# Performance work log

Hardware: AMD Instinct MI355X
Metric: run time of the kernel (lower is better)

The kernel has to match this reference:

```python
import jax, jax.numpy as jnp
import numpy as np

B, N, M, Q, H, D = 1, 512, 512, 128, 8, 16
CLIP = 10.0

def _xavier(key, shape):
    # xavier_uniform over last two dims (fan_in=Q, fan_out=D per head)
    fan_in, fan_out = shape[-2], shape[-1]
    limit = float(np.sqrt(6.0 / (fan_in + fan_out)))
    return jax.random.uniform(key, shape, jnp.float32, -limit, limit)

def setup_inputs() -> dict:
    key = jax.random.key(0)
    ks = jax.random.split(key, 12)
    return {
        "x": jax.random.normal(ks[0], (B, N, Q), jnp.float32),
        "y": jax.random.normal(ks[1], (B, M, Q), jnp.float32),
        "z": jax.random.normal(ks[2], (B, N, M, Q), jnp.float32),
        "mask": jax.random.randint(ks[3], (B, N, M), 0, 2, jnp.int32),
        "lambda_x": _xavier(ks[4], (H, Q, D)),
        "lambda_y": _xavier(ks[5], (H, Q, D)),
        "lambda_z1": _xavier(ks[6], (H, Q, D)),
        "lambda_z2": _xavier(ks[7], (H, Q, D)),
        "bias_lambda_x": jnp.zeros((H, D), jnp.float32),
        "bias_lambda_y": jnp.zeros((H, D), jnp.float32),
        "theta1": _xavier(ks[8], (H, Q, D)),
        "theta2": _xavier(ks[9], (H, Q, D)),
        "bias_theta": jnp.zeros((H, D), jnp.float32),
    }

def reference(x, y, z, mask, lambda_x, lambda_y, lambda_z1, lambda_z2,
              bias_lambda_x, bias_lambda_y, theta1, theta2, bias_theta):
    head_dim = lambda_x.shape[-1]
    # node projections: [B,N,H,D] / [B,M,H,D]
    r_x = jnp.einsum('bnq,hqd->bnhd', x, lambda_x) + bias_lambda_x
    r_y = jnp.einsum('bmq,hqd->bmhd', y, lambda_y) + bias_lambda_y
    # edge projections: [B,N,M,H,D]
    r_z1 = jnp.einsum('bnmq,hqd->bnmhd', z, lambda_z1)
    r_z2 = jnp.einsum('bnmq,hqd->bnmhd', z, lambda_z2)
    # broadcast-add node + edge terms, dot over D -> scores [B,H,N,M]
    att = jnp.einsum('bnmhd,bnmhd->bhnm',
                     r_x[:, :, None, :, :] + r_z1,
                     r_y[:, None, :, :, :] + r_z2)
    att = att * (head_dim ** -0.5)
    att = CLIP * jnp.tanh(att)
    att = jnp.where(mask[:, None, :, :] == 1, -jnp.inf, att)
    # NOTE: softmax over the N (source) axis, matching torch dim=-2
    w = jax.nn.softmax(att, axis=-2)
    x_p = jnp.einsum('bnq,hqd->bnhd', x, theta1)
    r = jnp.einsum('bhnm,bnhd->bmhd', w, x_p) + bias_theta
    return jnp.einsum('bmhd,hqd->bmq', r, theta2)
```

## Files before the change

### kernel.cpp

```cpp
#include <hip/hip_runtime.h>
#include <hip/hip_bf16.h>
#include <math.h>

typedef __attribute__((ext_vector_type(8))) short short8;
typedef __attribute__((ext_vector_type(4))) float f32x4;

#define NT 8

__global__ void pack_kernel(const float* __restrict__ lz1,
                            const float* __restrict__ lz2,
                            const float* __restrict__ th2,
                            const float* __restrict__ bth,
                            const float* __restrict__ lx,
                            const float* __restrict__ ly,
                            const float* __restrict__ t1,
                            __hip_bfloat16* __restrict__ Wh,
                            __hip_bfloat16* __restrict__ Wl,
                            float* __restrict__ T2,
                            float* __restrict__ ob,
                            float* __restrict__ Lp) {
    int tid = blockIdx.x * blockDim.x + threadIdx.x;
    int stride = gridDim.x * blockDim.x;
    for (int i = tid; i < 256 * 128; i += stride) {
        int op = i >> 7, q = i & 127;
        int h = op >> 5, wh = (op >> 4) & 1, d = op & 15;
        float v = (wh ? lz2 : lz1)[(h * 128 + q) * 16 + d];
        __hip_bfloat16 hb = __float2bfloat16(v);
        Wh[i] = hb;
        Wl[i] = __float2bfloat16(v - __bfloat162float(hb));
    }
    for (int i = tid; i < 128 * 128; i += stride) {
        int o = i >> 7, q = i & 127;
        int h = o >> 4, d = o & 15;
        T2[i] = th2[(h * 128 + q) * 16 + d];
    }
    for (int i = tid; i < 3 * 128 * 128; i += stride) {
        int which = i >> 14, q = (i >> 7) & 127, o = i & 127;
        int h = o >> 4, d = o & 15;
        const float* S = (which == 0) ? lx : (which == 1) ? ly : t1;
        Lp[i] = S[(h * 128 + q) * 16 + d];
    }
    if (tid < 128) {
        int q = tid;
        float s = 0.f;
#pragma unroll
        for (int h = 0; h < 8; ++h) {
#pragma unroll
            for (int c = 0; c < 4; ++c) {
                float4 a = *(const float4*)&bth[h * 16 + c * 4];
                float4 b = *(const float4*)&th2[(h * 128 + q) * 16 + c * 4];
                s += a.x * b.x + a.y * b.y + a.z * b.z + a.w * b.w;
            }
        }
        ob[q] = s;
    }
}

__global__ __launch_bounds__(128) void proj_kernel(const float* __restrict__ x,
                            const float* __restrict__ y,
                            const float* __restrict__ Lp,
                            const float* __restrict__ blx,
                            const float* __restrict__ bly,
                            float* __restrict__ rx,
                            float* __restrict__ ry,
                            float* __restrict__ xp) {
    __shared__ float rows[4][128];
    const int n0 = blockIdx.x * 4;
    const int which = blockIdx.y;
    const float* in = (which == 1) ? y : x;
    const float* L  = Lp + which * 16384;
    const int o = threadIdx.x;
#pragma unroll
    for (int j = 0; j < 4; ++j)
        rows[j][o] = in[(n0 + j) * 128 + o];
    __syncthreads();
    float acc[4] = {0.f, 0.f, 0.f, 0.f};
#pragma unroll 4
    for (int q = 0; q < 128; ++q) {
        float wv = L[q * 128 + o];
#pragma unroll
        for (int j = 0; j < 4; ++j)
            acc[j] = fmaf(rows[j][q], wv, acc[j]);
    }
    float b = (which == 0) ? blx[o] : (which == 1) ? bly[o] : 0.f;
    float* dst = (which == 0) ? rx : (which == 1) ? ry : xp;
#pragma unroll
    for (int j = 0; j < 4; ++j)
        dst[(n0 + j) * 128 + o] = acc[j] + b;
}

__global__ __launch_bounds__(256, 2) void big_kernel(
        const float* __restrict__ z,
        const int* __restrict__ mask,
        const __hip_bfloat16* __restrict__ Wh,
        const __hip_bfloat16* __restrict__ Wl,
        const float* __restrict__ rx,
        const float* __restrict__ ry,
        float* __restrict__ w) {
    __shared__ short zsh[2][64 * 128];
    __shared__ short zsl[2][64 * 128];
    const int m0 = blockIdx.x * 64;
    const int n0 = blockIdx.y * NT;
    const int tid = threadIdx.x;
    const int og = tid >> 6;
    const int l  = tid & 63;
    const int lg = l >> 4;
    const int lm = l & 15;

    const int srow = tid >> 2, kseg = tid & 3;
    const float* zbase = &z[(size_t)(m0 + srow) * 128 + kseg * 32];

    short8 bhr[2][4][2];
#pragma unroll
    for (int p = 0; p < 2; ++p)
#pragma unroll
        for (int ks = 0; ks < 4; ++ks)
#pragma unroll
            for (int j = 0; j < 2; ++j)
                bhr[p][ks][j] = *(const short8*)&Wh[(size_t)(og * 64 + (p * 2 + j) * 16 + lm) * 128 + ks * 32 + lg * 8];

    float4 ryr[2][4];
#pragma unroll
    for (int p = 0; p < 2; ++p)
#pragma unroll
        for (int i = 0; i < 4; ++i)
            ryr[p][i] = *(const float4*)&ry[(size_t)(m0 + i * 16 + lm) * 128 + (og * 2 + p) * 16 + lg * 4];

    float4 zr[8];
#define LOADZ(nn)                                                         \
    {                                                                     \
        const float* p_ = zbase + (size_t)(nn) * 65536;                   \
        _Pragma("unroll")                                                 \
        for (int c_ = 0; c_ < 8; ++c_) zr[c_] = *(const float4*)&p_[c_ * 4]; \
    }

#define CONVERT_WRITE(b)                                                  \
    {                                                                     \
        _Pragma("unroll")                                                 \
        for (int c8 = 0; c8 < 4; ++c8) {                                  \
            float vv[8] = {zr[2 * c8].x, zr[2 * c8].y, zr[2 * c8].z, zr[2 * c8].w, \
                           zr[2 * c8 + 1].x, zr[2 * c8 + 1].y, zr[2 * c8 + 1].z, zr[2 * c8 + 1].w}; \
            union { short8 s; __hip_bfloat16 h[8]; } uh, ul;              \
            _Pragma("unroll")                                             \
            for (int jj = 0; jj < 8; ++jj) {                              \
                float f_ = vv[jj];                                        \
                __hip_bfloat16 hb_ = __float2bfloat16(f_);                \
                uh.h[jj] = hb_;                                           \
                ul.h[jj] = __float2bfloat16(f_ - __bfloat162float(hb_));  \
            }                                                             \
            int cw_ = (kseg * 4 + c8) ^ (srow & 7);                       \
            *(short8*)&zsh[b][srow * 128 + cw_ * 8] = uh.s;               \
            *(short8*)&zsl[b][srow * 128 + cw_ * 8] = ul.s;               \
        }                                                                 \
    }

    LOADZ(n0);
    CONVERT_WRITE(0);
    LOADZ(n0 + 1);
    __syncthreads();

    for (int t = 0; t < NT; ++t) {
        const int n = n0 + t;
        const int cur = t & 1;
        const int mk = mask[n * 512 + m0 + l];

#pragma unroll
        for (int p = 0; p < 2; ++p) {
            const int h = og * 2 + p;
            f32x4 acc[4][2];
#pragma unroll
            for (int i = 0; i < 4; ++i) {
                acc[i][0] = (f32x4){0.f, 0.f, 0.f, 0.f};
                acc[i][1] = (f32x4){0.f, 0.f, 0.f, 0.f};
            }
#pragma unroll
            for (int ks = 0; ks < 4; ++ks) {
                short8 bl[2];
#pragma unroll
                for (int j = 0; j < 2; ++j)
                    bl[j] = *(const short8*)&Wl[(size_t)(og * 64 + (p * 2 + j) * 16 + lm) * 128 + ks * 32 + lg * 8];
                short8 ah[4], al[4];
#pragma unroll
                for (int i = 0; i < 4; ++i) {
                    int row = i * 16 + lm;
                    int cw = (ks * 4 + lg) ^ (row & 7);
                    ah[i] = *(const short8*)&zsh[cur][row * 128 + cw * 8];
                    al[i] = *(const short8*)&zsl[cur][row * 128 + cw * 8];
                }
#pragma unroll
                for (int i = 0; i < 4; ++i)
#pragma unroll
                    for (int j = 0; j < 2; ++j) {
                        acc[i][j] = __builtin_amdgcn_mfma_f32_16x16x32_bf16(bhr[p][ks][j], ah[i], acc[i][j], 0, 0, 0);
                        acc[i][j] = __builtin_amdgcn_mfma_f32_16x16x32_bf16(bhr[p][ks][j], al[i], acc[i][j], 0, 0, 0);
                        acc[i][j] = __builtin_amdgcn_mfma_f32_16x16x32_bf16(bl[j], ah[i], acc[i][j], 0, 0, 0);
                    }
            }

            float4 rxt = *(const float4*)&rx[n * 128 + h * 16 + lg * 4];
            const float rxv[4] = {rxt.x, rxt.y, rxt.z, rxt.w};
            float t4[4];
#pragma unroll
            for (int i = 0; i < 4; ++i) {
                const float ryv[4] = {ryr[p][i].x, ryr[p][i].y, ryr[p][i].z, ryr[p][i].w};
                float s = 0.f;
#pragma unroll
                for (int r = 0; r < 4; ++r)
                    s = fmaf(rxv[r] + acc[i][0][r], ryv[r] + acc[i][1][r], s);
                s += __shfl_xor(s, 16);
                s += __shfl_xor(s, 32);
                t4[i] = s;
            }
            float ta = (lg & 1) ? t4[1] : t4[0];
            float tb = (lg & 1) ? t4[3] : t4[2];
            float s  = (lg & 2) ? tb : ta;
            float e1 = __expf(0.5f * s);
            float wv = __expf(-20.f / (e1 + 1.f));
            if (mk == 1) wv = 0.f;
            w[((size_t)(h * 512 + n)) * 512 + m0 + l] = wv;
        }

        if (t + 1 < NT) {
            CONVERT_WRITE(cur ^ 1);
            if (t + 2 < NT) LOADZ(n0 + t + 2);
        }
        __syncthreads();
    }
#undef LOADZ
#undef CONVERT_WRITE
}

__global__ __launch_bounds__(256) void softpv_kernel(const float* __restrict__ w,
                                                     const float* __restrict__ xp,
                                                     float* __restrict__ rr) {
    __shared__ float xps[512][16];
    __shared__ float red[16][16][16];
    __shared__ float ssum[16][16];
    const int m0 = blockIdx.x * 16;
    const int h  = blockIdx.y;
    const int t  = threadIdx.x;
    const int ml = t & 15, g = t >> 4;

    for (int idx = t; idx < 512 * 4; idx += 256) {
        int nn = idx >> 2, c = idx & 3;
        *(float4*)&xps[nn][c * 4] = *(const float4*)&xp[nn * 128 + h * 16 + c * 4];
    }
    __syncthreads();

    const float* col = &w[((size_t)h * 512) * 512 + m0 + ml];
    float s = 0.f;
    float racc[16];
#pragma unroll
    for (int dd = 0; dd < 16; ++dd) racc[dd] = 0.f;
    for (int nn = g * 32; nn < g * 32 + 32; ++nn) {
        float e = col[(size_t)nn * 512];
        s += e;
#pragma unroll
        for (int c = 0; c < 4; ++c) {
            float4 xv = *(const float4*)&xps[nn][c * 4];
            racc[c * 4 + 0] = fmaf(e, xv.x, racc[c * 4 + 0]);
            racc[c * 4 + 1] = fmaf(e, xv.y, racc[c * 4 + 1]);
            racc[c * 4 + 2] = fmaf(e, xv.z, racc[c * 4 + 2]);
            racc[c * 4 + 3] = fmaf(e, xv.w, racc[c * 4 + 3]);
        }
    }
    ssum[g][ml] = s;
#pragma unroll
    for (int dd = 0; dd < 16; ++dd) red[g][ml][dd] = racc[dd];
    __syncthreads();

    {
        const int m = t & 15, dd = t >> 4;
        float stot = 0.f;
#pragma unroll
        for (int gg = 0; gg < 16; ++gg) stot += ssum[gg][m];
        float v = 0.f;
#pragma unroll
        for (int gg = 0; gg < 16; ++gg) v += red[gg][m][dd];
        rr[(size_t)(m0 + m) * 128 + h * 16 + dd] = v / stot;
    }
}

__global__ __launch_bounds__(128) void outg_kernel(const float* __restrict__ rr,
                            const float* __restrict__ T2,
                            const float* __restrict__ ob,
                            float* __restrict__ out) {
    __shared__ float rrow[4][128];
    const int m0 = blockIdx.x * 4;
    const int q = threadIdx.x;
#pragma unroll
    for (int j = 0; j < 4; ++j)
        rrow[j][q] = rr[(m0 + j) * 128 + q];
    __syncthreads();
    float acc[4] = {0.f, 0.f, 0.f, 0.f};
#pragma unroll 4
    for (int o = 0; o < 128; ++o) {
        float tv = T2[o * 128 + q];
#pragma unroll
        for (int j = 0; j < 4; ++j)
            acc[j] = fmaf(rrow[j][o], tv, acc[j]);
    }
    float b = ob[q];
#pragma unroll
    for (int j = 0; j < 4; ++j)
        out[(m0 + j) * 128 + q] = acc[j] + b;
}

extern "C" void kernel_launch(void* const* d_in, const int* in_sizes, int n_in,
                              void* d_out, int out_size, void* d_ws, size_t ws_size,
                              hipStream_t stream) {
    (void)in_sizes; (void)n_in; (void)out_size; (void)ws_size;
    const float* x   = (const float*)d_in[0];
    const float* y   = (const float*)d_in[1];
    const float* z   = (const float*)d_in[2];
    const int*  mask = (const int*)d_in[3];
    const float* lx  = (const float*)d_in[4];
    const float* ly  = (const float*)d_in[5];
    const float* lz1 = (const float*)d_in[6];
    const float* lz2 = (const float*)d_in[7];
    const float* blx = (const float*)d_in[8];
    const float* bly = (const float*)d_in[9];
    const float* t1  = (const float*)d_in[10];
    const float* t2  = (const float*)d_in[11];
    const float* bth = (const float*)d_in[12];
    float* out = (float*)d_out;

    float* ws = (float*)d_ws;
    float* rx = ws;
    float* ry = rx + 65536;
    float* xp = ry + 65536;
    __hip_bfloat16* Wh = (__hip_bfloat16*)(xp + 65536);
    __hip_bfloat16* Wl = (__hip_bfloat16*)(xp + 65536 + 16384);
    float* T2  = xp + 65536 + 32768;
    float* ob  = T2 + 16384;
    float* Lp  = ob + 128;
    float* wbuf= Lp + 49152;
    float* rr  = wbuf + 2097152;

    pack_kernel<<<dim3(32), dim3(256), 0, stream>>>(lz1, lz2, t2, bth, lx, ly, t1,
                                                    Wh, Wl, T2, ob, Lp);
    proj_kernel<<<dim3(128, 3), dim3(128), 0, stream>>>(x, y, Lp, blx, bly, rx, ry, xp);
    big_kernel<<<dim3(8, 64), dim3(256), 0, stream>>>(z, mask, Wh, Wl, rx, ry, wbuf);
    softpv_kernel<<<dim3(32, 8), dim3(256), 0, stream>>>(wbuf, xp, rr);
    outg_kernel<<<dim3(128), dim3(128), 0, stream>>>(rr, T2, ob, out);
}
```

Measured before the change: 303.7 us.

## Fuse pack/proj and softmax/output kernels, restructure big_kernel weight loads

Merges the weight pack and node projection kernels into one prep kernel that reads weights in their original layout, and merges the softmax-weighted reduction with the final theta2 projection into one finish kernel, cutting five launches to three. In big_kernel, the register-cached Wh fragments are dropped: both Wh and Wl are now loaded from global per k-step, and all four output tiles are computed in one pass. The launch bound's minimum-occupancy hint is removed. The finish kernel runs only 64 blocks and loops over heads serially, which may underuse the GPU, and the prep kernel's weight reads are strided.

```diff
diff --git a/kernel.cpp b/kernel.cpp
--- a/kernel.cpp
+++ b/kernel.cpp
@@ -7,89 +7,93 @@
 
 #define NT 8
 
-__global__ void pack_kernel(const float* __restrict__ lz1,
-                            const float* __restrict__ lz2,
-                            const float* __restrict__ th2,
-                            const float* __restrict__ bth,
-                            const float* __restrict__ lx,
-                            const float* __restrict__ ly,
-                            const float* __restrict__ t1,
-                            __hip_bfloat16* __restrict__ Wh,
-                            __hip_bfloat16* __restrict__ Wl,
-                            float* __restrict__ T2,
-                            float* __restrict__ ob,
-                            float* __restrict__ Lp) {
-    int tid = blockIdx.x * blockDim.x + threadIdx.x;
-    int stride = gridDim.x * blockDim.x;
-    for (int i = tid; i < 256 * 128; i += stride) {
-        int op = i >> 7, q = i & 127;
-        int h = op >> 5, wh = (op >> 4) & 1, d = op & 15;
-        float v = (wh ? lz2 : lz1)[(h * 128 + q) * 16 + d];
-        __hip_bfloat16 hb = __float2bfloat16(v);
-        Wh[i] = hb;
-        Wl[i] = __float2bfloat16(v - __bfloat162float(hb));
-    }
-    for (int i = tid; i < 128 * 128; i += stride) {
-        int o = i >> 7, q = i & 127;
-        int h = o >> 4, d = o & 15;
-        T2[i] = th2[(h * 128 + q) * 16 + d];
-    }
-    for (int i = tid; i < 3 * 128 * 128; i += stride) {
-        int which = i >> 14, q = (i >> 7) & 127, o = i & 127;
-        int h = o >> 4, d = o & 15;
-        const float* S = (which == 0) ? lx : (which == 1) ? ly : t1;
-        Lp[i] = S[(h * 128 + q) * 16 + d];
-    }
-    if (tid < 128) {
-        int q = tid;
-        float s = 0.f;
-#pragma unroll
-        for (int h = 0; h < 8; ++h) {
-#pragma unroll
-            for (int c = 0; c < 4; ++c) {
-                float4 a = *(const float4*)&bth[h * 16 + c * 4];
-                float4 b = *(const float4*)&th2[(h * 128 + q) * 16 + c * 4];
-                s += a.x * b.x + a.y * b.y + a.z * b.z + a.w * b.w;
-            }
-        }
-        ob[q] = s;
+__global__ __launch_bounds__(128) void prep_kernel(
+        const float* __restrict__ x,  const float* __restrict__ y,
+        const float* __restrict__ lx, const float* __restrict__ ly,
+        const float* __restrict__ t1,
+        const float* __restrict__ lz1, const float* __restrict__ lz2,
+        const float* __restrict__ th2, const float* __restrict__ bth,
+        const float* __restrict__ blx, const float* __restrict__ bly,
+        __hip_bfloat16* __restrict__ Wh, __hip_bfloat16* __restrict__ Wl,
+        float* __restrict__ T2, float* __restrict__ ob,
+        float* __restrict__ rx, float* __restrict__ ry, float* __restrict__ xp) {
+    const int bid = blockIdx.x;
+    const int t = threadIdx.x;
+    if (bid < 256) {
+        __shared__ float rows[4][128];
+        const int role = bid >> 7;
+        const int n0 = (bid & 127) * 4;
+        const float* in = role ? y : x;
+        const int o = t, h = o >> 4, d = o & 15;
+#pragma unroll
+        for (int j = 0; j < 4; ++j)
+            rows[j][o] = in[(n0 + j) * 128 + o];
+        __syncthreads();
+        if (role == 0) {
+            float a[4] = {0.f, 0.f, 0.f, 0.f}, b[4] = {0.f, 0.f, 0.f, 0.f};
+#pragma unroll 4
+            for (int q = 0; q < 128; ++q) {
+                float wa = lx[(h * 128 + q) * 16 + d];
+                float wb = t1[(h * 128 + q) * 16 + d];
+#pragma unroll
+                for (int j = 0; j < 4; ++j) {
+                    a[j] = fmaf(rows[j][q], wa, a[j]);
+                    b[j] = fmaf(rows[j][q], wb, b[j]);
+                }
+            }
+            float bx = blx[o];
+#pragma unroll
+            for (int j = 0; j < 4; ++j) {
+                rx[(n0 + j) * 128 + o] = a[j] + bx;
+                xp[(n0 + j) * 128 + o] = b[j];
+            }
+        } else {
+            float a[4] = {0.f, 0.f, 0.f, 0.f};
+#pragma unroll 4
+            for (int q = 0; q < 128; ++q) {
+                float wa = ly[(h * 128 + q) * 16 + d];
+#pragma unroll
+                for (int j = 0; j < 4; ++j)
+                    a[j] = fmaf(rows[j][q], wa, a[j]);
+            }
+            float by = bly[o];
+#pragma unroll
+            for (int j = 0; j < 4; ++j)
+                ry[(n0 + j) * 128 + o] = a[j] + by;
+        }
+    } else {
+        const int idx = (bid - 256) * 128 + t;
+#pragma unroll
+        for (int i = idx; i < 32768; i += 16384) {
+            int op = i >> 7, q = i & 127;
+            int h = op >> 5, wh = (op >> 4) & 1, d = op & 15;
+            float v = (wh ? lz2 : lz1)[(h * 128 + q) * 16 + d];
+            __hip_bfloat16 hb = __float2bfloat16(v);
+            Wh[i] = hb;
+            Wl[i] = __float2bfloat16(v - __bfloat162float(hb));
+        }
+        {
+            int o = idx >> 7, q = idx & 127;
+            int h = o >> 4, d = o & 15;
+            T2[idx] = th2[(h * 128 + q) * 16 + d];
+        }
+        if (idx < 128) {
+            int q = idx;
+            float s = 0.f;
+#pragma unroll
+            for (int h = 0; h < 8; ++h)
+#pragma unroll
+                for (int c = 0; c < 4; ++c) {
+                    float4 a = *(const float4*)&bth[h * 16 + c * 4];
+                    float4 b = *(const float4*)&th2[(h * 128 + q) * 16 + c * 4];
+                    s += a.x * b.x + a.y * b.y + a.z * b.z + a.w * b.w;
+                }
+            ob[q] = s;
+        }
     }
 }
 
-__global__ __launch_bounds__(128) void proj_kernel(const float* __restrict__ x,
-                            const float* __restrict__ y,
-                            const float* __restrict__ Lp,
-                            const float* __restrict__ blx,
-                            const float* __restrict__ bly,
-                            float* __restrict__ rx,
-                            float* __restrict__ ry,
-                            float* __restrict__ xp) {
-    __shared__ float rows[4][128];
-    const int n0 = blockIdx.x * 4;
-    const int which = blockIdx.y;
-    const float* in = (which == 1) ? y : x;
-    const float* L  = Lp + which * 16384;
-    const int o = threadIdx.x;
-#pragma unroll
-    for (int j = 0; j < 4; ++j)
-        rows[j][o] = in[(n0 + j) * 128 + o];
-    __syncthreads();
-    float acc[4] = {0.f, 0.f, 0.f, 0.f};
-#pragma unroll 4
-    for (int q = 0; q < 128; ++q) {
-        float wv = L[q * 128 + o];
-#pragma unroll
-        for (int j = 0; j < 4; ++j)
-            acc[j] = fmaf(rows[j][q], wv, acc[j]);
-    }
-    float b = (which == 0) ? blx[o] : (which == 1) ? bly[o] : 0.f;
-    float* dst = (which == 0) ? rx : (which == 1) ? ry : xp;
-#pragma unroll
-    for (int j = 0; j < 4; ++j)
-        dst[(n0 + j) * 128 + o] = acc[j] + b;
-}
-
-__global__ __launch_bounds__(256, 2) void big_kernel(
+__global__ __launch_bounds__(256) void big_kernel(
         const float* __restrict__ z,
         const int* __restrict__ mask,
         const __hip_bfloat16* __restrict__ Wh,
@@ -109,15 +113,6 @@
 
     const int srow = tid >> 2, kseg = tid & 3;
     const float* zbase = &z[(size_t)(m0 + srow) * 128 + kseg * 32];
-
-    short8 bhr[2][4][2];
-#pragma unroll
-    for (int p = 0; p < 2; ++p)
-#pragma unroll
-        for (int ks = 0; ks < 4; ++ks)
-#pragma unroll
-            for (int j = 0; j < 2; ++j)
-                bhr[p][ks][j] = *(const short8*)&Wh[(size_t)(og * 64 + (p * 2 + j) * 16 + lm) * 128 + ks * 32 + lg * 8];
 
     float4 ryr[2][4];
 #pragma unroll
@@ -164,39 +159,39 @@
         const int cur = t & 1;
         const int mk = mask[n * 512 + m0 + l];
 
+        f32x4 acc[4][4];
+#pragma unroll
+        for (int i = 0; i < 4; ++i)
+#pragma unroll
+            for (int pj = 0; pj < 4; ++pj) acc[i][pj] = (f32x4){0.f, 0.f, 0.f, 0.f};
+
+#pragma unroll
+        for (int ks = 0; ks < 4; ++ks) {
+            short8 ah[4], al[4];
+#pragma unroll
+            for (int i = 0; i < 4; ++i) {
+                int row = i * 16 + lm;
+                int cw = (ks * 4 + lg) ^ (row & 7);
+                ah[i] = *(const short8*)&zsh[cur][row * 128 + cw * 8];
+                al[i] = *(const short8*)&zsl[cur][row * 128 + cw * 8];
+            }
+#pragma unroll
+            for (int pj = 0; pj < 4; ++pj) {
+                size_t off = (size_t)(og * 64 + pj * 16 + lm) * 128 + ks * 32 + lg * 8;
+                short8 bh = *(const short8*)&Wh[off];
+                short8 bl = *(const short8*)&Wl[off];
+#pragma unroll
+                for (int i = 0; i < 4; ++i) {
+                    acc[i][pj] = __builtin_amdgcn_mfma_f32_16x16x32_bf16(bh, ah[i], acc[i][pj], 0, 0, 0);
+                    acc[i][pj] = __builtin_amdgcn_mfma_f32_16x16x32_bf16(bh, al[i], acc[i][pj], 0, 0, 0);
+                    acc[i][pj] = __builtin_amdgcn_mfma_f32_16x16x32_bf16(bl, ah[i], acc[i][pj], 0, 0, 0);
+                }
+            }
+        }
+
 #pragma unroll
         for (int p = 0; p < 2; ++p) {
             const int h = og * 2 + p;
-            f32x4 acc[4][2];
-#pragma unroll
-            for (int i = 0; i < 4; ++i) {
-                acc[i][0] = (f32x4){0.f, 0.f, 0.f, 0.f};
-                acc[i][1] = (f32x4){0.f, 0.f, 0.f, 0.f};
-            }
-#pragma unroll
-            for (int ks = 0; ks < 4; ++ks) {
-                short8 bl[2];
-#pragma unroll
-                for (int j = 0; j < 2; ++j)
-                    bl[j] = *(const short8*)&Wl[(size_t)(og * 64 + (p * 2 + j) * 16 + lm) * 128 + ks * 32 + lg * 8];
-                short8 ah[4], al[4];
-#pragma unroll
-                for (int i = 0; i < 4; ++i) {
-                    int row = i * 16 + lm;
-                    int cw = (ks * 4 + lg) ^ (row & 7);
-                    ah[i] = *(const short8*)&zsh[cur][row * 128 + cw * 8];
-                    al[i] = *(const short8*)&zsl[cur][row * 128 + cw * 8];
-                }
-#pragma unroll
-                for (int i = 0; i < 4; ++i)
-#pragma unroll
-                    for (int j = 0; j < 2; ++j) {
-                        acc[i][j] = __builtin_amdgcn_mfma_f32_16x16x32_bf16(bhr[p][ks][j], ah[i], acc[i][j], 0, 0, 0);
-                        acc[i][j] = __builtin_amdgcn_mfma_f32_16x16x32_bf16(bhr[p][ks][j], al[i], acc[i][j], 0, 0, 0);
-                        acc[i][j] = __builtin_amdgcn_mfma_f32_16x16x32_bf16(bl[j], ah[i], acc[i][j], 0, 0, 0);
-                    }
-            }
-
             float4 rxt = *(const float4*)&rx[n * 128 + h * 16 + lg * 4];
             const float rxv[4] = {rxt.x, rxt.y, rxt.z, rxt.w};
             float t4[4];
@@ -206,7 +201,7 @@
                 float s = 0.f;
 #pragma unroll
                 for (int r = 0; r < 4; ++r)
-                    s = fmaf(rxv[r] + acc[i][0][r], ryv[r] + acc[i][1][r], s);
+                    s = fmaf(rxv[r] + acc[i][p * 2][r], ryv[r] + acc[i][p * 2 + 1][r], s);
                 s += __shfl_xor(s, 16);
                 s += __shfl_xor(s, 32);
                 t4[i] = s;
@@ -230,80 +225,84 @@
 #undef CONVERT_WRITE
 }
 
-__global__ __launch_bounds__(256) void softpv_kernel(const float* __restrict__ w,
-                                                     const float* __restrict__ xp,
-                                                     float* __restrict__ rr) {
+__global__ __launch_bounds__(256) void finish_kernel(
+        const float* __restrict__ w,
+        const float* __restrict__ xp,
+        const float* __restrict__ T2,
+        const float* __restrict__ ob,
+        float* __restrict__ out) {
     __shared__ float xps[512][16];
-    __shared__ float red[16][16][16];
-    __shared__ float ssum[16][16];
-    const int m0 = blockIdx.x * 16;
-    const int h  = blockIdx.y;
+    __shared__ float red[32][8][16];
+    __shared__ float ssum[32][8];
+    __shared__ float rrs[8][128];
+    const int m0 = blockIdx.x * 8;
     const int t  = threadIdx.x;
-    const int ml = t & 15, g = t >> 4;
-
-    for (int idx = t; idx < 512 * 4; idx += 256) {
-        int nn = idx >> 2, c = idx & 3;
-        *(float4*)&xps[nn][c * 4] = *(const float4*)&xp[nn * 128 + h * 16 + c * 4];
-    }
-    __syncthreads();
-
-    const float* col = &w[((size_t)h * 512) * 512 + m0 + ml];
-    float s = 0.f;
-    float racc[16];
-#pragma unroll
-    for (int dd = 0; dd < 16; ++dd) racc[dd] = 0.f;
-    for (int nn = g * 32; nn < g * 32 + 32; ++nn) {
-        float e = col[(size_t)nn * 512];
-        s += e;
-#pragma unroll
-        for (int c = 0; c < 4; ++c) {
-            float4 xv = *(const float4*)&xps[nn][c * 4];
-            racc[c * 4 + 0] = fmaf(e, xv.x, racc[c * 4 + 0]);
-            racc[c * 4 + 1] = fmaf(e, xv.y, racc[c * 4 + 1]);
-            racc[c * 4 + 2] = fmaf(e, xv.z, racc[c * 4 + 2]);
-            racc[c * 4 + 3] = fmaf(e, xv.w, racc[c * 4 + 3]);
-        }
-    }
-    ssum[g][ml] = s;
-#pragma unroll
-    for (int dd = 0; dd < 16; ++dd) red[g][ml][dd] = racc[dd];
-    __syncthreads();
+    const int ml = t & 7, g = t >> 3;
+
+    for (int h = 0; h < 8; ++h) {
+        for (int idx = t; idx < 512 * 4; idx += 256) {
+            int nn = idx >> 2, c = idx & 3;
+            *(float4*)&xps[nn][c * 4] = *(const float4*)&xp[nn * 128 + h * 16 + c * 4];
+        }
+        __syncthreads();
+
+        const float* col = &w[((size_t)h * 512) * 512 + m0 + ml];
+        float s = 0.f;
+        float racc[16];
+#pragma unroll
+        for (int dd = 0; dd < 16; ++dd) racc[dd] = 0.f;
+        for (int nn = g * 16; nn < g * 16 + 16; ++nn) {
+            float e = col[(size_t)nn * 512];
+            s += e;
+#pragma unroll
+            for (int c = 0; c < 4; ++c) {
+                float4 xv = *(const float4*)&xps[nn][c * 4];
+                racc[c * 4 + 0] = fmaf(e, xv.x, racc[c * 4 + 0]);
+                racc[c * 4 + 1] = fmaf(e, xv.y, racc[c * 4 + 1]);
+                racc[c * 4 + 2] = fmaf(e, xv.z, racc[c * 4 + 2]);
+                racc[c * 4 + 3] = fmaf(e, xv.w, racc[c * 4 + 3]);
+            }
+        }
+        ssum[g][ml] = s;
+#pragma unroll
+        for (int dd = 0; dd < 16; ++dd) red[g][ml][dd] = racc[dd];
+        __syncthreads();
+
+        if (t < 128) {
+            const int m = t & 7, dd = t >> 3;
+            float stot = 0.f;
+#pragma unroll
+            for (int gg = 0; gg < 32; ++gg) stot += ssum[gg][m];
+            float v = 0.f;
+#pragma unroll
+            for (int gg = 0; gg < 32; ++gg) v += red[gg][m][dd];
+            rrs[m][h * 16 + dd] = v / stot;
+        }
+        __syncthreads();
+    }
 
     {
-        const int m = t & 15, dd = t >> 4;
-        float stot = 0.f;
-#pragma unroll
-        for (int gg = 0; gg < 16; ++gg) stot += ssum[gg][m];
-        float v = 0.f;
-#pragma unroll
-        for (int gg = 0; gg < 16; ++gg) v += red[gg][m][dd];
-        rr[(size_t)(m0 + m) * 128 + h * 16 + dd] = v / stot;
-    }
-}
-
-__global__ __launch_bounds__(128) void outg_kernel(const float* __restrict__ rr,
-                            const float* __restrict__ T2,
-                            const float* __restrict__ ob,
-                            float* __restrict__ out) {
-    __shared__ float rrow[4][128];
-    const int m0 = blockIdx.x * 4;
-    const int q = threadIdx.x;
-#pragma unroll
-    for (int j = 0; j < 4; ++j)
-        rrow[j][q] = rr[(m0 + j) * 128 + q];
-    __syncthreads();
-    float acc[4] = {0.f, 0.f, 0.f, 0.f};
-#pragma unroll 4
-    for (int o = 0; o < 128; ++o) {
-        float tv = T2[o * 128 + q];
+        const int q = t & 127, mg = t >> 7;
+        float acc4[4] = {0.f, 0.f, 0.f, 0.f};
+        for (int o4 = 0; o4 < 32; ++o4) {
+            float tv[4];
+#pragma unroll
+            for (int k = 0; k < 4; ++k)
+                tv[k] = T2[(o4 * 4 + k) * 128 + q];
+#pragma unroll
+            for (int j = 0; j < 4; ++j) {
+                float4 rv = *(const float4*)&rrs[mg * 4 + j][o4 * 4];
+                acc4[j] = fmaf(rv.x, tv[0], acc4[j]);
+                acc4[j] = fmaf(rv.y, tv[1], acc4[j]);
+                acc4[j] = fmaf(rv.z, tv[2], acc4[j]);
+                acc4[j] = fmaf(rv.w, tv[3], acc4[j]);
+            }
+        }
+        float b = ob[q];
 #pragma unroll
         for (int j = 0; j < 4; ++j)
-            acc[j] = fmaf(rrow[j][o], tv, acc[j]);
-    }
-    float b = ob[q];
-#pragma unroll
-    for (int j = 0; j < 4; ++j)
-        out[(m0 + j) * 128 + q] = acc[j] + b;
+            out[(m0 + mg * 4 + j) * 128 + q] = acc4[j] + b;
+    }
 }
 
 extern "C" void kernel_launch(void* const* d_in, const int* in_sizes, int n_in,
@@ -333,14 +332,11 @@
     __hip_bfloat16* Wl = (__hip_bfloat16*)(xp + 65536 + 16384);
     float* T2  = xp + 65536 + 32768;
     float* ob  = T2 + 16384;
-    float* Lp  = ob + 128;
-    float* wbuf= Lp + 49152;
-    float* rr  = wbuf + 2097152;
-
-    pack_kernel<<<dim3(32), dim3(256), 0, stream>>>(lz1, lz2, t2, bth, lx, ly, t1,
-                                                    Wh, Wl, T2, ob, Lp);
-    proj_kernel<<<dim3(128, 3), dim3(128), 0, stream>>>(x, y, Lp, blx, bly, rx, ry, xp);
+    float* wbuf= ob + 128;
+
+    prep_kernel<<<dim3(384), dim3(128), 0, stream>>>(
+        x, y, lx, ly, t1, lz1, lz2, t2, bth, blx, bly,
+        Wh, Wl, T2, ob, rx, ry, xp);
     big_kernel<<<dim3(8, 64), dim3(256), 0, stream>>>(z, mask, Wh, Wl, rx, ry, wbuf);
-    softpv_kernel<<<dim3(32, 8), dim3(256), 0, stream>>>(wbuf, xp, rr);
-    outg_kernel<<<dim3(128), dim3(128), 0, stream>>>(rr, T2, ob, out);
+    finish_kernel<<<dim3(64), dim3(256), 0, stream>>>(wbuf, xp, T2, ob, out);
 }
```

New measurement: 297.7 us. -2.0%, faster.
